# Kernel tuning notes

Hardware: AMD Instinct MI355X
Metric: run time of the kernel (lower is better)

The kernel has to match this reference:

```python
import jax, jax.numpy as jnp
import numpy as np

NUM_LEVELS = 16
FEATS_PER_LEVEL = 2
LOG2_HASHMAP = 19
TABLE_SIZE = 1 << LOG2_HASHMAP
BASE_RES = 16
DESIRED_RES = 4096
PER_LEVEL_SCALE = float(np.exp(np.log(DESIRED_RES / BASE_RES) / (NUM_LEVELS - 1)))
PRIMES = (np.uint32(1), np.uint32(2654435761), np.uint32(805459861))
N_POINTS = 2_000_000


def _level_features(x, table, level):
    # x: [N,3] in [0,1]; table: [TABLE_SIZE, F]
    scale = BASE_RES * (PER_LEVEL_SCALE ** level) - 1.0
    res = int(np.ceil(scale)) + 1
    dense = (res ** 3) <= TABLE_SIZE  # tcnn uses dense indexing when grid fits
    pos = x * scale + 0.5
    pos0 = jnp.floor(pos)
    w = pos - pos0                     # trilinear weights, [N,3]
    base = pos0.astype(jnp.uint32)
    out = jnp.zeros((x.shape[0], table.shape[1]), dtype=table.dtype)
    for c in range(8):                 # 8 corners of the voxel
        offs = [(c >> d) & 1 for d in range(3)]
        pc = [jnp.minimum(base[:, d] + np.uint32(offs[d]), np.uint32(res - 1)) for d in range(3)]
        if dense:
            idx = pc[0] + pc[1] * np.uint32(res) + pc[2] * np.uint32(res * res)
        else:
            idx = (pc[0] * PRIMES[0]) ^ (pc[1] * PRIMES[1]) ^ (pc[2] * PRIMES[2])
            idx = idx & np.uint32(TABLE_SIZE - 1)
        wt = jnp.ones(x.shape[0], dtype=x.dtype)
        for d in range(3):
            wt = wt * (w[:, d] if offs[d] else (1.0 - w[:, d]))
        out = out + wt[:, None] * table[idx.astype(jnp.int32)]
    return out


def hashgrid_encode(x, tables):
    # x: [N,3] in [0,1]; tables: [L, TABLE_SIZE, F] -> [N, L*F]
    return jnp.concatenate(
        [_level_features(x, tables[l], l) for l in range(NUM_LEVELS)], axis=-1)


def setup_inputs() -> dict:
    key = jax.random.key(0)
    k1, k2, k3, k4, k5 = jax.random.split(key, 5)
    points = jax.random.uniform(k1, (N_POINTS, 3), dtype=jnp.float32)
    # tcnn hashgrid init: uniform(-1e-4, 1e-4)
    tables = jax.random.uniform(k2, (NUM_LEVELS, TABLE_SIZE, FEATS_PER_LEVEL),
                                minval=-1e-4, maxval=1e-4, dtype=jnp.float32)
    def kaiming(k, fan_out, fan_in):
        bound = np.sqrt(2.0) * np.sqrt(3.0 / fan_in)
        return jax.random.uniform(k, (fan_out, fan_in), minval=-bound, maxval=bound,
                                  dtype=jnp.float32)
    W1 = kaiming(k3, 32, 32)
    W2 = kaiming(k4, 32, 32)
    W3 = kaiming(k5, 4, 32)
    aabb = jnp.stack([jnp.zeros(3, jnp.float32), jnp.ones(3, jnp.float32)])
    return {"points": points, "tables": tables, "W1": W1, "W2": W2, "W3": W3,
            "aabb": aabb}


def reference(points, tables, W1, W2, W3, aabb):
    texc = jnp.clip((points - aabb[0][None, :]) / (aabb[1] - aabb[0])[None, :], 0.0, 1.0)
    enc = hashgrid_encode(texc, tables)            # [N, 32]
    h = jax.nn.relu(enc @ W1.T)
    h = jax.nn.relu(h @ W2.T)
    out = h @ W3.T                                 # [N, 4]
    mn = jnp.array([0.0, 0.0, 0.0, 0.01], dtype=out.dtype)
    mx = jnp.array([1.0, 1.0, 1.0, 1.0], dtype=out.dtype)
    return jax.nn.sigmoid(out) * (mx - mn) + mn
```

## Files before the change

kernel.cpp:

```cpp
#include <hip/hip_runtime.h>
#include <cmath>


namespace {
constexpr int kLevels = 16;
constexpr unsigned kTableSize = 1u << 19;
constexpr unsigned kMask = kTableSize - 1u;
constexpr int kNumCells = 1 << 15;
constexpr int kHistBlocks = 64;
constexpr int kHistEntries = kNumCells * kHistBlocks;
constexpr int kScan1Blocks = kHistEntries / 256;
constexpr int kScan2Blocks = kScan1Blocks / 256;

typedef _Float16 half2_t __attribute__((ext_vector_type(2)));
typedef unsigned int u32;

struct LevelParams {
  float scale[kLevels];
  unsigned res[kLevels];
  int dense[kLevels];
};
}

__device__ __forceinline__ u32 part1by2(u32 x) {
  x &= 0x3FFu;
  x = (x | (x << 16)) & 0x030000FFu;
  x = (x | (x << 8))  & 0x0300F00Fu;
  x = (x | (x << 4))  & 0x030C30C3u;
  x = (x | (x << 2))  & 0x09249249u;
  return x;
}

__device__ __forceinline__ u32 cell_of(float x, float y, float z) {
  u32 cx = min((u32)(x * 32.f), 31u);
  u32 cy = min((u32)(y * 32.f), 31u);
  u32 cz = min((u32)(z * 32.f), 31u);
  return part1by2(cx) | (part1by2(cy) << 1) | (part1by2(cz) << 2);
}

__global__ __launch_bounds__(256)
void conv_tables_kernel(const float2* __restrict__ src, half2_t* __restrict__ dst,
                        int n_entries,
                        const float* __restrict__ W1, const float* __restrict__ W2,
                        const float* __restrict__ W3, half2_t* __restrict__ Wh)
{
  int i = blockIdx.x * blockDim.x + threadIdx.x;
  if (i < 512) {
    Wh[i] = half2_t{(_Float16)W1[2 * i], (_Float16)W1[2 * i + 1]};
  } else if (i < 1024) {
    int t = i - 512;
    Wh[512 + t] = half2_t{(_Float16)W2[2 * t], (_Float16)W2[2 * t + 1]};
  } else if (i < 1088) {
    int t = i - 1024;
    Wh[1024 + t] = half2_t{(_Float16)W3[2 * t], (_Float16)W3[2 * t + 1]};
  }
  int stride = gridDim.x * blockDim.x;
  for (; i < n_entries; i += stride) {
    float2 v = src[i];
    dst[i] = half2_t{(_Float16)v.x, (_Float16)v.y};
  }
}

__global__ __launch_bounds__(256)
void hist_pack_kernel(const float* __restrict__ points, const float* __restrict__ aabb,
                      u32* __restrict__ hist, u32* __restrict__ cr, int n, int ppb)
{
  __shared__ u32 h[kNumCells / 2];
  int t = threadIdx.x;
  int b = blockIdx.x;
  #pragma unroll
  for (int j = t; j < kNumCells / 2; j += 256) h[j] = 0u;
  __syncthreads();

  float a0x = aabb[0], a0y = aabb[1], a0z = aabb[2];
  float a1x = aabb[3], a1y = aabb[4], a1z = aabb[5];
  int start = b * ppb;
  int end = min(start + ppb, n);
  for (int i = start + t; i < end; i += 256) {
    float x = fminf(fmaxf((points[3 * i + 0] - a0x) / (a1x - a0x), 0.f), 1.f);
    float y = fminf(fmaxf((points[3 * i + 1] - a0y) / (a1y - a0y), 0.f), 1.f);
    float z = fminf(fmaxf((points[3 * i + 2] - a0z) / (a1z - a0z), 0.f), 1.f);
    u32 c = cell_of(x, y, z);
    u32 sh = (c & 1u) * 16u;
    u32 old = atomicAdd(&h[c >> 1], 1u << sh);
    u32 rank = (old >> sh) & 0xFFFFu;
    cr[i] = c | (rank << 15);
  }
  __syncthreads();
  for (int j = t; j < kNumCells; j += 256) {
    u32 cnt = (h[j >> 1] >> ((j & 1u) * 16u)) & 0xFFFFu;
    hist[(size_t)j * kHistBlocks + b] = cnt;
  }
}

__global__ __launch_bounds__(256)
void scan_block_kernel(u32* __restrict__ data, u32* __restrict__ sums)
{
  __shared__ u32 s[256];
  int t = threadIdx.x;
  int base = blockIdx.x * 256;
  u32 v = data[base + t];
  s[t] = v;
  __syncthreads();
  #pragma unroll
  for (int off = 1; off < 256; off <<= 1) {
    u32 a = (t >= off) ? s[t - off] : 0u;
    __syncthreads();
    s[t] += a;
    __syncthreads();
  }
  if (t == 255) sums[blockIdx.x] = s[255];
  data[base + t] = s[t] - v;
}

__global__ __launch_bounds__(64)
void scan_small_kernel(u32* __restrict__ d, int m)
{
  if (threadIdx.x == 0) {
    u32 acc = 0;
    for (int j = 0; j < m; ++j) { u32 v = d[j]; d[j] = acc; acc += v; }
  }
}

__global__ __launch_bounds__(256)
void add_offsets_kernel(u32* __restrict__ data, const u32* __restrict__ sums)
{
  data[blockIdx.x * 256 + threadIdx.x] += sums[blockIdx.x];
}

__global__ __launch_bounds__(256)
void scatter_kernel(const float* __restrict__ points, const float* __restrict__ aabb,
                    const u32* __restrict__ hist, const u32* __restrict__ cr,
                    float4* __restrict__ sp, int n, int ppb)
{
  int i = blockIdx.x * blockDim.x + threadIdx.x;
  if (i >= n) return;
  float a0x = aabb[0], a0y = aabb[1], a0z = aabb[2];
  float a1x = aabb[3], a1y = aabb[4], a1z = aabb[5];
  float x = fminf(fmaxf((points[3 * i + 0] - a0x) / (a1x - a0x), 0.f), 1.f);
  float y = fminf(fmaxf((points[3 * i + 1] - a0y) / (a1y - a0y), 0.f), 1.f);
  float z = fminf(fmaxf((points[3 * i + 2] - a0z) / (a1z - a0z), 0.f), 1.f);
  u32 v = cr[i];
  u32 c = v & 0x7FFFu;
  u32 rank = v >> 15;
  int b = i / ppb;
  u32 pos = hist[(size_t)c * kHistBlocks + b] + rank;
  sp[pos] = make_float4(x, y, z, __uint_as_float((u32)i));
}

__device__ __forceinline__ u32 sel4(uint4 v, u32 j) {
  u32 lo = (j & 1u) ? v.y : v.x;
  u32 hi = (j & 1u) ? v.w : v.z;
  return (j & 2u) ? hi : lo;
}

__global__ __launch_bounds__(256)
void encode_sorted_kernel(const float4* __restrict__ sp,
                          const u32* __restrict__ tables,
                          half2_t* __restrict__ enc,
                          LevelParams lp, int n, int bpl)
{
  int l = blockIdx.x / bpl;
  int i = (blockIdx.x - l * bpl) * blockDim.x + threadIdx.x;
  if (i >= n) return;

  float4 c = sp[i];
  float x = c.x, y = c.y, z = c.z;

  float s = lp.scale[l];
  unsigned res = lp.res[l];
  bool dense = (lp.dense[l] != 0);
  unsigned rm1 = res - 1u;
  unsigned res2 = res * res;
  const u32* tab = tables + (size_t)l * kTableSize;

  float fx = x * s + 0.5f, fy = y * s + 0.5f, fz = z * s + 0.5f;
  float fx0 = floorf(fx), fy0 = floorf(fy), fz0 = floorf(fz);
  float wx = fx - fx0, wy = fy - fy0, wz = fz - fz0;
  unsigned bx = (unsigned)fx0, by = (unsigned)fy0, bz = (unsigned)fz0;

  unsigned pcx0 = min(bx, rm1), pcx1 = min(bx + 1u, rm1);

  u32 idx0[4], idx1[4];
  #pragma unroll
  for (int p = 0; p < 4; ++p) {
    unsigned oy = (unsigned)(p & 1);
    unsigned oz = (unsigned)(p >> 1);
    unsigned pcy = min(by + oy, rm1);
    unsigned pcz = min(bz + oz, rm1);
    if (dense) {
      u32 bb = pcy * res + pcz * res2;
      idx0[p] = pcx0 + bb;
      idx1[p] = pcx1 + bb;
    } else {
      u32 h = (pcy * 2654435761u) ^ (pcz * 805459861u);
      idx0[p] = (pcx0 ^ h) & kMask;
      idx1[p] = (pcx1 ^ h) & kMask;
    }
  }

  uint4 v[4];
  #pragma unroll
  for (int p = 0; p < 4; ++p)
    v[p] = *reinterpret_cast<const uint4*>(tab + (idx0[p] & ~3u));

  u32 e1x[4] = {0u, 0u, 0u, 0u};
  #pragma unroll
  for (int p = 0; p < 4; ++p) {
    if ((idx0[p] ^ idx1[p]) >= 4u) e1x[p] = tab[idx1[p]];
  }

  float wx1 = wx, wx0 = 1.f - wx;
  float acc0 = 0.f, acc1 = 0.f;
  #pragma unroll
  for (int p = 0; p < 4; ++p) {
    unsigned oy = (unsigned)(p & 1);
    unsigned oz = (unsigned)(p >> 1);
    float wyz = (oy ? wy : 1.f - wy) * (oz ? wz : 1.f - wz);
    u32 e0 = sel4(v[p], idx0[p] & 3u);
    u32 e1g = sel4(v[p], idx1[p] & 3u);
    u32 e1 = ((idx0[p] ^ idx1[p]) < 4u) ? e1g : e1x[p];
    half2_t f0 = __builtin_bit_cast(half2_t, e0);
    half2_t f1 = __builtin_bit_cast(half2_t, e1);
    float w0 = wyz * wx0, w1 = wyz * wx1;
    acc0 += w0 * (float)f0.x + w1 * (float)f1.x;
    acc1 += w0 * (float)f0.y + w1 * (float)f1.y;
  }
  enc[(size_t)l * n + i] = half2_t{(_Float16)acc0, (_Float16)acc1};
}

__device__ __forceinline__ float dot2_acc(half2_t a, half2_t b, float c) {
#if __has_builtin(__builtin_amdgcn_fdot2)
  return __builtin_amdgcn_fdot2(a, b, c, false);
#else
  return c + (float)a.x * (float)b.x + (float)a.y * (float)b.y;
#endif
}

__global__ __launch_bounds__(256)
void mlp_kernel(const half2_t* __restrict__ enc,
                const half2_t* __restrict__ Wh,
                const float4* __restrict__ sp,
                float* __restrict__ out, int n)
{
  int i = blockIdx.x * blockDim.x + threadIdx.x;
  if (i >= n) return;

  half2_t e[16];
  #pragma unroll
  for (int l = 0; l < kLevels; ++l) e[l] = enc[(size_t)l * n + i];

  const half2_t* W1h = Wh;
  const half2_t* W2h = Wh + 512;
  const half2_t* W3h = Wh + 1024;

  float h1f[32];
  #pragma unroll
  for (int j = 0; j < 32; ++j) {
    float acc = 0.f;
    #pragma unroll
    for (int k = 0; k < 16; ++k) acc = dot2_acc(e[k], W1h[16 * j + k], acc);
    h1f[j] = fmaxf(acc, 0.f);
  }
  half2_t h1[16];
  #pragma unroll
  for (int k = 0; k < 16; ++k)
    h1[k] = half2_t{(_Float16)h1f[2 * k], (_Float16)h1f[2 * k + 1]};

  float h2f[32];
  #pragma unroll
  for (int j = 0; j < 32; ++j) {
    float acc = 0.f;
    #pragma unroll
    for (int k = 0; k < 16; ++k) acc = dot2_acc(h1[k], W2h[16 * j + k], acc);
    h2f[j] = fmaxf(acc, 0.f);
  }
  half2_t h2[16];
  #pragma unroll
  for (int k = 0; k < 16; ++k)
    h2[k] = half2_t{(_Float16)h2f[2 * k], (_Float16)h2f[2 * k + 1]};

  float o[4];
  #pragma unroll
  for (int j = 0; j < 4; ++j) {
    float acc = 0.f;
    #pragma unroll
    for (int k = 0; k < 16; ++k) acc = dot2_acc(h2[k], W3h[16 * j + k], acc);
    o[j] = acc;
  }

  float4 r;
  r.x = 1.f / (1.f + __expf(-o[0]));
  r.y = 1.f / (1.f + __expf(-o[1]));
  r.z = 1.f / (1.f + __expf(-o[2]));
  r.w = 0.99f / (1.f + __expf(-o[3])) + 0.01f;
  int oi = sp ? (int)__float_as_uint(sp[i].w) : i;
  reinterpret_cast<float4*>(out)[oi] = r;
}

__global__ __launch_bounds__(256)
void encode_raw_kernel(const float* __restrict__ points,
                       const u32* __restrict__ tables,
                       const float* __restrict__ aabb,
                       half2_t* __restrict__ enc,
                       LevelParams lp, int n, int bpl)
{
  int l = blockIdx.x / bpl;
  int i = (blockIdx.x - l * bpl) * blockDim.x + threadIdx.x;
  if (i >= n) return;

  float a0x = aabb[0], a0y = aabb[1], a0z = aabb[2];
  float a1x = aabb[3], a1y = aabb[4], a1z = aabb[5];
  float x = fminf(fmaxf((points[3 * i + 0] - a0x) / (a1x - a0x), 0.f), 1.f);
  float y = fminf(fmaxf((points[3 * i + 1] - a0y) / (a1y - a0y), 0.f), 1.f);
  float z = fminf(fmaxf((points[3 * i + 2] - a0z) / (a1z - a0z), 0.f), 1.f);

  float s = lp.scale[l];
  unsigned res = lp.res[l];
  bool dense = (lp.dense[l] != 0);
  unsigned rm1 = res - 1u;
  unsigned res2 = res * res;
  const u32* tab = tables + (size_t)l * kTableSize;

  float fx = x * s + 0.5f, fy = y * s + 0.5f, fz = z * s + 0.5f;
  float fx0 = floorf(fx), fy0 = floorf(fy), fz0 = floorf(fz);
  float wx = fx - fx0, wy = fy - fy0, wz = fz - fz0;
  unsigned bx = (unsigned)fx0, by = (unsigned)fy0, bz = (unsigned)fz0;
  unsigned pcx0 = min(bx, rm1), pcx1 = min(bx + 1u, rm1);

  u32 idx0[4], idx1[4];
  #pragma unroll
  for (int p = 0; p < 4; ++p) {
    unsigned oy = (unsigned)(p & 1);
    unsigned oz = (unsigned)(p >> 1);
    unsigned pcy = min(by + oy, rm1);
    unsigned pcz = min(bz + oz, rm1);
    if (dense) {
      u32 bb = pcy * res + pcz * res2;
      idx0[p] = pcx0 + bb;
      idx1[p] = pcx1 + bb;
    } else {
      u32 h = (pcy * 2654435761u) ^ (pcz * 805459861u);
      idx0[p] = (pcx0 ^ h) & kMask;
      idx1[p] = (pcx1 ^ h) & kMask;
    }
  }
  uint4 v[4];
  #pragma unroll
  for (int p = 0; p < 4; ++p)
    v[p] = *reinterpret_cast<const uint4*>(tab + (idx0[p] & ~3u));
  u32 e1x[4] = {0u, 0u, 0u, 0u};
  #pragma unroll
  for (int p = 0; p < 4; ++p) {
    if ((idx0[p] ^ idx1[p]) >= 4u) e1x[p] = tab[idx1[p]];
  }
  float wx1 = wx, wx0 = 1.f - wx;
  float acc0 = 0.f, acc1 = 0.f;
  #pragma unroll
  for (int p = 0; p < 4; ++p) {
    unsigned oy = (unsigned)(p & 1);
    unsigned oz = (unsigned)(p >> 1);
    float wyz = (oy ? wy : 1.f - wy) * (oz ? wz : 1.f - wz);
    u32 e0 = sel4(v[p], idx0[p] & 3u);
    u32 e1g = sel4(v[p], idx1[p] & 3u);
    u32 e1 = ((idx0[p] ^ idx1[p]) < 4u) ? e1g : e1x[p];
    half2_t f0 = __builtin_bit_cast(half2_t, e0);
    half2_t f1 = __builtin_bit_cast(half2_t, e1);
    float w0 = wyz * wx0, w1 = wyz * wx1;
    acc0 += w0 * (float)f0.x + w1 * (float)f1.x;
    acc1 += w0 * (float)f0.y + w1 * (float)f1.y;
  }
  enc[(size_t)l * n + i] = half2_t{(_Float16)acc0, (_Float16)acc1};
}

__global__ __launch_bounds__(256)
void hashgrid_mlp_kernel(const float* __restrict__ points,
                         const float* __restrict__ tables,
                         const float* __restrict__ W1,
                         const float* __restrict__ W2,
                         const float* __restrict__ W3,
                         const float* __restrict__ aabb,
                         float* __restrict__ out,
                         LevelParams lp, int n)
{
  int i = blockIdx.x * blockDim.x + threadIdx.x;
  if (i >= n) return;
  float a0x = aabb[0], a0y = aabb[1], a0z = aabb[2];
  float a1x = aabb[3], a1y = aabb[4], a1z = aabb[5];
  float x = fminf(fmaxf((points[3 * i + 0] - a0x) / (a1x - a0x), 0.f), 1.f);
  float y = fminf(fmaxf((points[3 * i + 1] - a0y) / (a1y - a0y), 0.f), 1.f);
  float z = fminf(fmaxf((points[3 * i + 2] - a0z) / (a1z - a0z), 0.f), 1.f);
  float enc[2 * kLevels];
  #pragma unroll
  for (int l = 0; l < kLevels; ++l) {
    float s = lp.scale[l];
    unsigned res = lp.res[l];
    bool dense = (lp.dense[l] != 0);
    unsigned rm1 = res - 1u;
    unsigned res2 = res * res;
    float fx = x * s + 0.5f, fy = y * s + 0.5f, fz = z * s + 0.5f;
    float fx0 = floorf(fx), fy0 = floorf(fy), fz0 = floorf(fz);
    float wx = fx - fx0, wy = fy - fy0, wz = fz - fz0;
    unsigned bx = (unsigned)fx0, by = (unsigned)fy0, bz = (unsigned)fz0;
    const float2* tab = reinterpret_cast<const float2*>(tables) + (size_t)l * kTableSize;
    float acc0 = 0.f, acc1 = 0.f;
    #pragma unroll
    for (int c = 0; c < 8; ++c) {
      unsigned ox = (unsigned)(c & 1);
      unsigned oy = (unsigned)((c >> 1) & 1);
      unsigned oz = (unsigned)((c >> 2) & 1);
      unsigned pcx = min(bx + ox, rm1);
      unsigned pcy = min(by + oy, rm1);
      unsigned pcz = min(bz + oz, rm1);
      unsigned idx;
      if (dense) idx = pcx + pcy * res + pcz * res2;
      else idx = (pcx ^ (pcy * 2654435761u) ^ (pcz * 805459861u)) & kMask;
      float wt = (ox ? wx : 1.f - wx) * (oy ? wy : 1.f - wy) * (oz ? wz : 1.f - wz);
      float2 f = tab[idx];
      acc0 += wt * f.x;
      acc1 += wt * f.y;
    }
    enc[2 * l + 0] = acc0;
    enc[2 * l + 1] = acc1;
  }
  float h1[32];
  #pragma unroll
  for (int j = 0; j < 32; ++j) {
    float acc = 0.f;
    #pragma unroll
    for (int k = 0; k < 32; ++k) acc += enc[k] * W1[32 * j + k];
    h1[j] = fmaxf(acc, 0.f);
  }
  float h2[32];
  #pragma unroll
  for (int j = 0; j < 32; ++j) {
    float acc = 0.f;
    #pragma unroll
    for (int k = 0; k < 32; ++k) acc += h1[k] * W2[32 * j + k];
    h2[j] = fmaxf(acc, 0.f);
  }
  float o[4];
  #pragma unroll
  for (int j = 0; j < 4; ++j) {
    float acc = 0.f;
    #pragma unroll
    for (int k = 0; k < 32; ++k) acc += h2[k] * W3[32 * j + k];
    o[j] = acc;
  }
  float4 r;
  r.x = 1.f / (1.f + __expf(-o[0]));
  r.y = 1.f / (1.f + __expf(-o[1]));
  r.z = 1.f / (1.f + __expf(-o[2]));
  r.w = 0.99f / (1.f + __expf(-o[3])) + 0.01f;
  reinterpret_cast<float4*>(out)[i] = r;
}

extern "C" void kernel_launch(void* const* d_in, const int* in_sizes, int n_in,
                              void* d_out, int out_size, void* d_ws, size_t ws_size,
                              hipStream_t stream) {
  const float* points = (const float*)d_in[0];
  const float* tables = (const float*)d_in[1];
  const float* W1     = (const float*)d_in[2];
  const float* W2     = (const float*)d_in[3];
  const float* W3     = (const float*)d_in[4];
  const float* aabb   = (const float*)d_in[5];
  float* out = (float*)d_out;
  int n = in_sizes[0] / 3;

  LevelParams lp;
  const double pls = std::exp(std::log(4096.0 / 16.0) / 15.0);
  for (int l = 0; l < kLevels; ++l) {
    double s = 16.0 * std::pow(pls, (double)l) - 1.0;
    lp.scale[l] = (float)s;
    long long res = (long long)std::ceil(s) + 1;
    lp.res[l] = (unsigned)res;
    lp.dense[l] = (res * res * res <= (long long)kTableSize) ? 1 : 0;
  }

  const int block = 256;
  const int n_entries = kLevels * (int)kTableSize;
  const int grid_n = (n + block - 1) / block;
  const int ppb = (n + kHistBlocks - 1) / kHistBlocks;

  auto align256 = [](size_t v) { return (v + 255) & ~(size_t)255; };
  const size_t tab_b   = align256((size_t)n_entries * 4);
  const size_t enc_b   = align256((size_t)kLevels * n * 4);
  const size_t wh_b    = align256(1088 * 4);
  const size_t sp_b    = align256((size_t)n * 16);
  const size_t cr_b    = align256((size_t)n * 4);
  const size_t hist_b  = align256((size_t)kHistEntries * 4);
  const size_t sumA_b  = align256((size_t)kScan1Blocks * 4);
  const size_t sumB_b  = align256((size_t)kScan2Blocks * 4);
  const size_t bin_need = cr_b + hist_b + sumA_b + sumB_b;
  const size_t need_sorted = tab_b + enc_b + wh_b + sp_b;
  const size_t need_r3     = tab_b + enc_b + wh_b;

  if (ws_size >= need_sorted && bin_need <= enc_b && ppb < (1 << 15)) {
    char* p = (char*)d_ws;
    half2_t* tab_f16 = (half2_t*)p;            p += tab_b;
    char*    enc_rgn = p;                      p += enc_b;
    half2_t* Wh      = (half2_t*)p;            p += wh_b;
    float4*  sp      = (float4*)p;

    half2_t* enc = (half2_t*)enc_rgn;
    u32* cr   = (u32*)enc_rgn;
    u32* hist = (u32*)(enc_rgn + cr_b);
    u32* sumA = (u32*)(enc_rgn + cr_b + hist_b);
    u32* sumB = (u32*)(enc_rgn + cr_b + hist_b + sumA_b);

    conv_tables_kernel<<<4096, block, 0, stream>>>(
        reinterpret_cast<const float2*>(tables), tab_f16, n_entries, W1, W2, W3, Wh);

    hist_pack_kernel<<<kHistBlocks, block, 0, stream>>>(points, aabb, hist, cr, n, ppb);
    scan_block_kernel<<<kScan1Blocks, 256, 0, stream>>>(hist, sumA);
    scan_block_kernel<<<kScan2Blocks, 256, 0, stream>>>(sumA, sumB);
    scan_small_kernel<<<1, 64, 0, stream>>>(sumB, kScan2Blocks);
    add_offsets_kernel<<<kScan2Blocks, 256, 0, stream>>>(sumA, sumB);
    add_offsets_kernel<<<kScan1Blocks, 256, 0, stream>>>(hist, sumA);
    scatter_kernel<<<grid_n, block, 0, stream>>>(points, aabb, hist, cr, sp, n, ppb);

    encode_sorted_kernel<<<grid_n * kLevels, block, 0, stream>>>(
        sp, reinterpret_cast<const u32*>(tab_f16), enc, lp, n, grid_n);

    mlp_kernel<<<grid_n, block, 0, stream>>>(enc, Wh, sp, out, n);
  } else if (ws_size >= need_r3) {
    char* p = (char*)d_ws;
    half2_t* tab_f16 = (half2_t*)p;            p += tab_b;
    half2_t* enc     = (half2_t*)p;            p += enc_b;
    half2_t* Wh      = (half2_t*)p;

    conv_tables_kernel<<<4096, block, 0, stream>>>(
        reinterpret_cast<const float2*>(tables), tab_f16, n_entries, W1, W2, W3, Wh);
    encode_raw_kernel<<<grid_n * kLevels, block, 0, stream>>>(
        points, reinterpret_cast<const u32*>(tab_f16), aabb, enc, lp, n, grid_n);
    mlp_kernel<<<grid_n, block, 0, stream>>>(enc, Wh, nullptr, out, n);
  } else {
    hashgrid_mlp_kernel<<<grid_n, block, 0, stream>>>(
        points, tables, W1, W2, W3, aabb, out, lp, n);
  }
}
```

Measured before the change: 876.7 us.

## Raise histogram block count and switch to row-major hist with column-chunked scan

Raises the number of histogram blocks from 64 to 512 so the binning pass has far more parallelism, and stores per-block counts row-major (block, cell). The offset computation becomes a per-cell column reduction over 4 chunks of 128 rows, a scan over the 32K cell totals, and then a per-column exclusive scan. Global memory traffic for the histogram grows about 8x (16M entries) and more small kernels are launched. The ppb limit is tightened to match the 16-bit in-LDS counters.

After: 830.4 us. 1.06x faster.

```diff
diff --git a/kernel.cpp b/kernel.cpp
--- a/kernel.cpp
+++ b/kernel.cpp
@@ -7,10 +7,9 @@
 constexpr unsigned kTableSize = 1u << 19;
 constexpr unsigned kMask = kTableSize - 1u;
 constexpr int kNumCells = 1 << 15;
-constexpr int kHistBlocks = 64;
+constexpr int kHistBlocks = 512;
+constexpr int kChunkRows = 128;
 constexpr int kHistEntries = kNumCells * kHistBlocks;
-constexpr int kScan1Blocks = kHistEntries / 256;
-constexpr int kScan2Blocks = kScan1Blocks / 256;
 
 typedef _Float16 half2_t __attribute__((ext_vector_type(2)));
 typedef unsigned int u32;
@@ -68,7 +67,6 @@
   __shared__ u32 h[kNumCells / 2];
   int t = threadIdx.x;
   int b = blockIdx.x;
-  #pragma unroll
   for (int j = t; j < kNumCells / 2; j += 256) h[j] = 0u;
   __syncthreads();
 
@@ -87,10 +85,31 @@
     cr[i] = c | (rank << 15);
   }
   __syncthreads();
+  u32* row = hist + (size_t)b * kNumCells;
   for (int j = t; j < kNumCells; j += 256) {
     u32 cnt = (h[j >> 1] >> ((j & 1u) * 16u)) & 0xFFFFu;
-    hist[(size_t)j * kHistBlocks + b] = cnt;
-  }
+    row[j] = cnt;
+  }
+}
+
+__global__ __launch_bounds__(256)
+void colsum4_kernel(const u32* __restrict__ hist, u32* __restrict__ partial)
+{
+  int chunk = blockIdx.x >> 7;
+  int c = (blockIdx.x & 127) * 256 + threadIdx.x;
+  const u32* row = hist + (size_t)chunk * kChunkRows * kNumCells + c;
+  u32 acc = 0;
+  #pragma unroll 4
+  for (int b = 0; b < kChunkRows; ++b) acc += row[(size_t)b * kNumCells];
+  partial[chunk * kNumCells + c] = acc;
+}
+
+__global__ __launch_bounds__(256)
+void combine_kernel(const u32* __restrict__ partial, u32* __restrict__ colsum)
+{
+  int c = blockIdx.x * 256 + threadIdx.x;
+  colsum[c] = partial[c] + partial[kNumCells + c] +
+              partial[2 * kNumCells + c] + partial[3 * kNumCells + c];
 }
 
 __global__ __launch_bounds__(256)
@@ -126,6 +145,34 @@
 void add_offsets_kernel(u32* __restrict__ data, const u32* __restrict__ sums)
 {
   data[blockIdx.x * 256 + threadIdx.x] += sums[blockIdx.x];
+}
+
+__global__ __launch_bounds__(256)
+void base_kernel(u32* __restrict__ partial, const u32* __restrict__ colsum)
+{
+  int c = blockIdx.x * 256 + threadIdx.x;
+  u32 p0 = partial[c];
+  u32 p1 = partial[kNumCells + c];
+  u32 p2 = partial[2 * kNumCells + c];
+  u32 b0 = colsum[c];
+  partial[c] = b0;
+  partial[kNumCells + c] = b0 + p0;
+  partial[2 * kNumCells + c] = b0 + p0 + p1;
+  partial[3 * kNumCells + c] = b0 + p0 + p1 + p2;
+}
+
+__global__ __launch_bounds__(256)
+void colscan4_kernel(u32* __restrict__ hist, const u32* __restrict__ partial)
+{
+  int chunk = blockIdx.x >> 7;
+  int c = (blockIdx.x & 127) * 256 + threadIdx.x;
+  u32 acc = partial[chunk * kNumCells + c];
+  u32* row = hist + (size_t)chunk * kChunkRows * kNumCells + c;
+  for (int b = 0; b < kChunkRows; ++b) {
+    u32 v = row[(size_t)b * kNumCells];
+    row[(size_t)b * kNumCells] = acc;
+    acc += v;
+  }
 }
 
 __global__ __launch_bounds__(256)
@@ -144,7 +191,7 @@
   u32 c = v & 0x7FFFu;
   u32 rank = v >> 15;
   int b = i / ppb;
-  u32 pos = hist[(size_t)c * kHistBlocks + b] + rank;
+  u32 pos = hist[(size_t)b * kNumCells + c] + rank;
   sp[pos] = make_float4(x, y, z, __uint_as_float((u32)i));
 }
 
@@ -489,13 +536,14 @@
   const size_t sp_b    = align256((size_t)n * 16);
   const size_t cr_b    = align256((size_t)n * 4);
   const size_t hist_b  = align256((size_t)kHistEntries * 4);
-  const size_t sumA_b  = align256((size_t)kScan1Blocks * 4);
-  const size_t sumB_b  = align256((size_t)kScan2Blocks * 4);
-  const size_t bin_need = cr_b + hist_b + sumA_b + sumB_b;
+  const size_t part_b  = align256((size_t)4 * kNumCells * 4);
+  const size_t col_b   = align256((size_t)kNumCells * 4);
+  const size_t sum_b   = align256((size_t)(kNumCells / 256) * 4);
+  const size_t bin_need = cr_b + hist_b + part_b + col_b + sum_b;
   const size_t need_sorted = tab_b + enc_b + wh_b + sp_b;
   const size_t need_r3     = tab_b + enc_b + wh_b;
 
-  if (ws_size >= need_sorted && bin_need <= enc_b && ppb < (1 << 15)) {
+  if (ws_size >= need_sorted && bin_need <= enc_b && ppb < (1 << 12)) {
     char* p = (char*)d_ws;
     half2_t* tab_f16 = (half2_t*)p;            p += tab_b;
     char*    enc_rgn = p;                      p += enc_b;
@@ -503,20 +551,23 @@
     float4*  sp      = (float4*)p;
 
     half2_t* enc = (half2_t*)enc_rgn;
-    u32* cr   = (u32*)enc_rgn;
-    u32* hist = (u32*)(enc_rgn + cr_b);
-    u32* sumA = (u32*)(enc_rgn + cr_b + hist_b);
-    u32* sumB = (u32*)(enc_rgn + cr_b + hist_b + sumA_b);
+    u32* cr      = (u32*)enc_rgn;
+    u32* hist    = (u32*)(enc_rgn + cr_b);
+    u32* partial = (u32*)(enc_rgn + cr_b + hist_b);
+    u32* colsum  = (u32*)(enc_rgn + cr_b + hist_b + part_b);
+    u32* sums    = (u32*)(enc_rgn + cr_b + hist_b + part_b + col_b);
 
     conv_tables_kernel<<<4096, block, 0, stream>>>(
         reinterpret_cast<const float2*>(tables), tab_f16, n_entries, W1, W2, W3, Wh);
 
     hist_pack_kernel<<<kHistBlocks, block, 0, stream>>>(points, aabb, hist, cr, n, ppb);
-    scan_block_kernel<<<kScan1Blocks, 256, 0, stream>>>(hist, sumA);
-    scan_block_kernel<<<kScan2Blocks, 256, 0, stream>>>(sumA, sumB);
-    scan_small_kernel<<<1, 64, 0, stream>>>(sumB, kScan2Blocks);
-    add_offsets_kernel<<<kScan2Blocks, 256, 0, stream>>>(sumA, sumB);
-    add_offsets_kernel<<<kScan1Blocks, 256, 0, stream>>>(hist, sumA);
+    colsum4_kernel<<<512, block, 0, stream>>>(hist, partial);
+    combine_kernel<<<kNumCells / 256, block, 0, stream>>>(partial, colsum);
+    scan_block_kernel<<<kNumCells / 256, block, 0, stream>>>(colsum, sums);
+    scan_small_kernel<<<1, 64, 0, stream>>>(sums, kNumCells / 256);
+    add_offsets_kernel<<<kNumCells / 256, block, 0, stream>>>(colsum, sums);
+    base_kernel<<<kNumCells / 256, block, 0, stream>>>(partial, colsum);
+    colscan4_kernel<<<512, block, 0, stream>>>(hist, partial);
     scatter_kernel<<<grid_n, block, 0, stream>>>(points, aabb, hist, cr, sp, n, ppb);
 
     encode_sorted_kernel<<<grid_n * kLevels, block, 0, stream>>>(
```
